# Kernel optimization log

Hardware: AMD Instinct MI355X
Metric: run time of the kernel (lower is better)

## Reference

```python
import jax, jax.numpy as jnp
import numpy as np


def setup_inputs() -> dict:
    key = jax.random.key(0)
    k1, k2, k3, k4 = jax.random.split(key, 4)
    N, F, E = 131072, 512, 256
    x = jax.random.normal(k1, (N, F), dtype=jnp.float32)
    W = jax.random.normal(k2, (E, F), dtype=jnp.float32) * 0.05  # stacked weak-classifier weights
    b = jax.random.normal(k3, (E,), dtype=jnp.float32) * 0.05
    alphas = jax.random.normal(k4, (E,), dtype=jnp.float32)
    return {"x": x, "W": W, "b": b, "alphas": alphas}


def reference(x, W, b, alphas):
    # Fused version of the per-estimator Python loop:
    # per estimator e: pred_e = round(sigmoid(x @ W[e] + b[e])) in {0,1}
    logits = jnp.einsum('nf,ef->ne', x, W) + b              # [N, E]
    preds = jnp.round(jax.nn.sigmoid(logits))               # [N, E], half-to-even like torch.round
    # original casts each (alpha * pred) term to long (trunc toward zero) before accumulating
    terms = jnp.trunc(alphas[None, :] * preds)              # [N, E]
    acc = jnp.sum(terms, axis=1)                            # [N]
    return jnp.sign(acc)
```

## Files before the change

### kernel.cpp

```cpp
#include <hip/hip_runtime.h>
#include <math.h>


#define F_DIM  512
#define BM     128
#define BK     32
#define KSTEPS 16
#define NT     8
#define WSLOTS 256
#define TAU    1e-3f

typedef float f32x4  __attribute__((ext_vector_type(4)));
typedef short bf16x8 __attribute__((ext_vector_type(8)));

__device__ inline unsigned short bf16_rne(float v) {
    unsigned u = __float_as_uint(v);
    u += 0x7FFFu + ((u >> 16) & 1u);
    return (unsigned short)(u >> 16);
}
__device__ inline float bf16_to_f32(unsigned short h) {
    return __uint_as_float(((unsigned)h) << 16);
}

__device__ inline void cvt8(const f32x4 a, const f32x4 b, bf16x8& hi, bf16x8& lo) {
    #pragma unroll
    for (int j = 0; j < 4; ++j) {
        const float v0 = a[j], v1 = b[j];
        const unsigned short h0 = bf16_rne(v0);
        const unsigned short h1 = bf16_rne(v1);
        hi[j]     = (short)h0;
        hi[j + 4] = (short)h1;
        lo[j]     = (short)bf16_rne(v0 - bf16_to_f32(h0));
        lo[j + 4] = (short)bf16_rne(v1 - bf16_to_f32(h1));
    }
}

__device__ __attribute__((noinline)) bool exact_pred(const float* __restrict__ xr,
                                                     const float* __restrict__ wr,
                                                     float bv) {
    double s0 = 0.0, s1 = 0.0, s2 = 0.0, s3 = 0.0;
    for (int k = 0; k < F_DIM; k += 4) {
        s0 = fma((double)xr[k + 0], (double)wr[k + 0], s0);
        s1 = fma((double)xr[k + 1], (double)wr[k + 1], s1);
        s2 = fma((double)xr[k + 2], (double)wr[k + 2], s2);
        s3 = fma((double)xr[k + 3], (double)wr[k + 3], s3);
    }
    double s = ((s0 + s1) + (s2 + s3)) + (double)bv;
    return s > 0.0;
}

__global__ __launch_bounds__(256)
void ada_prep(const float* __restrict__ W, const float* __restrict__ alphas,
              unsigned short* __restrict__ wfrag) {
    __shared__ int se[WSLOTS];
    __shared__ int wcnt[4];
    const int tid = threadIdx.x;

    se[tid] = 0;
    __syncthreads();
    const float t = truncf(alphas[tid]);
    const bool flag = (t != 0.0f);
    const unsigned long long m64 = __ballot(flag);
    const int lane = tid & 63, wvi = tid >> 6;
    if (lane == 0) wcnt[wvi] = __popcll(m64);
    __syncthreads();
    int off = 0;
    #pragma unroll
    for (int w = 0; w < 4; ++w) if (w < wvi) off += wcnt[w];
    if (flag) se[off + __popcll(m64 & ((1ull << lane) - 1ull))] = tid;
    __syncthreads();

    const int job = blockIdx.x * 256 + tid;
    const int jl  = job & 63;
    const int t8  = (job >> 6) & 7;
    const int ks  = (job >> 9) & 15;
    const int p   = (job >> 13) & 1;
    const int col = p * 128 + t8 * 16 + (jl & 15);
    const int k   = ks * 32 + (jl >> 4) * 8;

    const float* src = W + (size_t)se[col] * F_DIM + k;
    const f32x4 a = *(const f32x4*)(src);
    const f32x4 b = *(const f32x4*)(src + 4);
    bf16x8 hi, lo;
    cvt8(a, b, hi, lo);

    const size_t base = ((((size_t)(p * 16 + ks) * 8 + t8) * 2 + 0) * 64 + jl) * 8;
    *(bf16x8*)(wfrag + base)       = hi;
    *(bf16x8*)(wfrag + base + 512) = lo;
}

__global__ __launch_bounds__(256, 2)
void ada_mfma4(const float* __restrict__ x, const float* __restrict__ W,
               const float* __restrict__ bias, const float* __restrict__ alphas,
               const unsigned short* __restrict__ wfrag,
               float* __restrict__ out) {
    __shared__ unsigned short wbuf[2][8192];
    __shared__ int   se[WSLOTS];
    __shared__ float st[WSLOTS];
    __shared__ float sb[WSLOTS];
    __shared__ int   wcnt[4];

    const int tid = threadIdx.x;
    const int n0  = blockIdx.x * BM;

    se[tid] = 0; st[tid] = 0.0f; sb[tid] = 0.0f;
    __syncthreads();
    const float t = truncf(alphas[tid]);
    const bool flag = (t != 0.0f);
    const unsigned long long m64 = __ballot(flag);
    const int lane = tid & 63, wv = tid >> 6;
    if (lane == 0) wcnt[wv] = __popcll(m64);
    __syncthreads();
    int off = 0;
    #pragma unroll
    for (int w = 0; w < 4; ++w) if (w < wv) off += wcnt[w];
    const int M = wcnt[0] + wcnt[1] + wcnt[2] + wcnt[3];
    if (flag) {
        const int slot = off + __popcll(m64 & ((1ull << lane) - 1ull));
        se[slot] = tid; st[slot] = t; sb[slot] = bias[tid];
    }
    __syncthreads();

    const int quad = (tid >> 4) & 3;
    const int l15  = tid & 15;
    const int rw   = wv * 32;

    const float* xp0 = x + (size_t)(n0 + rw + l15) * F_DIM + quad * 8;
    const float* xp1 = xp0 + (size_t)16 * F_DIM;

    int part[2][4];
    #pragma unroll
    for (int mt = 0; mt < 2; ++mt)
        #pragma unroll
        for (int r = 0; r < 4; ++r) part[mt][r] = 0;

    for (int cb = 0; cb < M; cb += 128) {
        const unsigned short* wsp = wfrag + (size_t)(cb >> 7) * KSTEPS * 8192;

        f32x4 acc[2][NT];
        #pragma unroll
        for (int mt = 0; mt < 2; ++mt)
            #pragma unroll
            for (int nt = 0; nt < NT; ++nt)
                acc[mt][nt] = (f32x4){0.0f, 0.0f, 0.0f, 0.0f};

        {
            const unsigned short* gs = wsp + wv * 2048 + lane * 8;
            unsigned short* lb = &wbuf[0][wv * 2048];
            #pragma unroll
            for (int i = 0; i < 4; ++i)
                __builtin_amdgcn_global_load_lds(
                    (const __attribute__((address_space(1))) void*)(gs + i * 512),
                    (__attribute__((address_space(3))) void*)(lb + i * 512),
                    16, 0, 0);
        }
        f32x4 xv0 = *(const f32x4*)(xp0);
        f32x4 xv1 = *(const f32x4*)(xp0 + 4);
        f32x4 xv2 = *(const f32x4*)(xp1);
        f32x4 xv3 = *(const f32x4*)(xp1 + 4);
        __syncthreads();

        #pragma unroll
        for (int ks = 0; ks < KSTEPS; ++ks) {
            const int cur = ks & 1;

            f32x4 xn0, xn1, xn2, xn3;
            if (ks + 1 < KSTEPS) {
                const unsigned short* gs = wsp + (size_t)(ks + 1) * 8192 + wv * 2048 + lane * 8;
                unsigned short* lb = &wbuf[cur ^ 1][wv * 2048];
                #pragma unroll
                for (int i = 0; i < 4; ++i)
                    __builtin_amdgcn_global_load_lds(
                        (const __attribute__((address_space(1))) void*)(gs + i * 512),
                        (__attribute__((address_space(3))) void*)(lb + i * 512),
                        16, 0, 0);
                const int kf = (ks + 1) * BK;
                xn0 = *(const f32x4*)(xp0 + kf);
                xn1 = *(const f32x4*)(xp0 + kf + 4);
                xn2 = *(const f32x4*)(xp1 + kf);
                xn3 = *(const f32x4*)(xp1 + kf + 4);
            }

            bf16x8 ah0, al0, ah1, al1;
            cvt8(xv0, xv1, ah0, al0);
            cvt8(xv2, xv3, ah1, al1);

            const unsigned short* wb = wbuf[cur];
            #pragma unroll
            for (int nt = 0; nt < NT; ++nt) {
                const bf16x8 bh = *(const bf16x8*)&wb[(nt * 2 + 0) * 512 + lane * 8];
                const bf16x8 bl = *(const bf16x8*)&wb[(nt * 2 + 1) * 512 + lane * 8];
                acc[0][nt] = __builtin_amdgcn_mfma_f32_16x16x32_bf16(ah0, bh, acc[0][nt], 0, 0, 0);
                acc[1][nt] = __builtin_amdgcn_mfma_f32_16x16x32_bf16(ah1, bh, acc[1][nt], 0, 0, 0);
                acc[0][nt] = __builtin_amdgcn_mfma_f32_16x16x32_bf16(al0, bh, acc[0][nt], 0, 0, 0);
                acc[1][nt] = __builtin_amdgcn_mfma_f32_16x16x32_bf16(al1, bh, acc[1][nt], 0, 0, 0);
                acc[0][nt] = __builtin_amdgcn_mfma_f32_16x16x32_bf16(ah0, bl, acc[0][nt], 0, 0, 0);
                acc[1][nt] = __builtin_amdgcn_mfma_f32_16x16x32_bf16(ah1, bl, acc[1][nt], 0, 0, 0);
            }

            __syncthreads();

            if (ks + 1 < KSTEPS) { xv0 = xn0; xv1 = xn1; xv2 = xn2; xv3 = xn3; }
        }

        #pragma unroll
        for (int nt = 0; nt < NT; ++nt) {
            const int col = cb + nt * 16 + l15;
            const float tv = st[col];
            if (tv != 0.0f) {
                const float bv = sb[col];
                const int it = (int)tv;
                #pragma unroll
                for (int mt = 0; mt < 2; ++mt) {
                    #pragma unroll
                    for (int r = 0; r < 4; ++r) {
                        const float logit = acc[mt][nt][r] + bv;
                        bool pred = (logit > 0.0f);
                        if (fabsf(logit) < TAU) {
                            const int row = rw + mt * 16 + quad * 4 + r;
                            pred = exact_pred(x + (size_t)(n0 + row) * F_DIM,
                                              W + (size_t)se[col] * F_DIM, bv);
                        }
                        if (pred) part[mt][r] += it;
                    }
                }
            }
        }
    }

    #pragma unroll
    for (int mt = 0; mt < 2; ++mt) {
        #pragma unroll
        for (int r = 0; r < 4; ++r) {
            int v = part[mt][r];
            v += __shfl_xor(v, 1);
            v += __shfl_xor(v, 2);
            v += __shfl_xor(v, 4);
            v += __shfl_xor(v, 8);
            part[mt][r] = v;
        }
    }
    if (l15 == 0) {
        #pragma unroll
        for (int mt = 0; mt < 2; ++mt) {
            float4 o;
            o.x = (part[mt][0] > 0) ? 1.0f : (part[mt][0] < 0 ? -1.0f : 0.0f);
            o.y = (part[mt][1] > 0) ? 1.0f : (part[mt][1] < 0 ? -1.0f : 0.0f);
            o.z = (part[mt][2] > 0) ? 1.0f : (part[mt][2] < 0 ? -1.0f : 0.0f);
            o.w = (part[mt][3] > 0) ? 1.0f : (part[mt][3] < 0 ? -1.0f : 0.0f);
            *(float4*)(out + n0 + rw + mt * 16 + quad * 4) = o;
        }
    }
}

extern "C" void kernel_launch(void* const* d_in, const int* in_sizes, int n_in,
                              void* d_out, int out_size, void* d_ws, size_t ws_size,
                              hipStream_t stream) {
    const float* x      = (const float*)d_in[0];
    const float* W      = (const float*)d_in[1];
    const float* bias   = (const float*)d_in[2];
    const float* alphas = (const float*)d_in[3];
    float* out = (float*)d_out;

    const int n = in_sizes[0] / F_DIM;
    const int nblocks = n / BM;

    unsigned short* wfrag = (unsigned short*)d_ws;

    ada_prep<<<dim3(64), dim3(256), 0, stream>>>(W, alphas, wfrag);
    ada_mfma4<<<dim3(nblocks), dim3(256), 0, stream>>>(x, W, bias, alphas, wfrag, out);
}
```

Measured before the change: 549.7 us.

## Defer near-threshold exact recomputation to a separate fixup kernel via record list

Instead of calling a noinline double-precision dot product inline in the GEMM epilogue when a logit is near zero, the main kernel now writes raw integer votes and appends ambiguous (row, estimator, pred) records through an atomic counter. A separate fixup kernel recomputes those records exactly and corrects votes atomically, and a final kernel applies sign. This removes divergence and register pressure from the hot kernel, at the cost of two extra launches, global atomics, and a capped record buffer that could drop corrections if overflowed. The x bf16 conversion is also moved to the loop top to simplify the prefetch registers.

```diff
diff --git a/kernel.cpp b/kernel.cpp
--- a/kernel.cpp
+++ b/kernel.cpp
@@ -9,6 +9,7 @@
 #define NT     8
 #define WSLOTS 256
 #define TAU    1e-3f
+#define RECCAP 65536
 
 typedef float f32x4  __attribute__((ext_vector_type(4)));
 typedef short bf16x8 __attribute__((ext_vector_type(8)));
@@ -35,26 +36,14 @@
     }
 }
 
-__device__ __attribute__((noinline)) bool exact_pred(const float* __restrict__ xr,
-                                                     const float* __restrict__ wr,
-                                                     float bv) {
-    double s0 = 0.0, s1 = 0.0, s2 = 0.0, s3 = 0.0;
-    for (int k = 0; k < F_DIM; k += 4) {
-        s0 = fma((double)xr[k + 0], (double)wr[k + 0], s0);
-        s1 = fma((double)xr[k + 1], (double)wr[k + 1], s1);
-        s2 = fma((double)xr[k + 2], (double)wr[k + 2], s2);
-        s3 = fma((double)xr[k + 3], (double)wr[k + 3], s3);
-    }
-    double s = ((s0 + s1) + (s2 + s3)) + (double)bv;
-    return s > 0.0;
-}
-
 __global__ __launch_bounds__(256)
 void ada_prep(const float* __restrict__ W, const float* __restrict__ alphas,
-              unsigned short* __restrict__ wfrag) {
+              unsigned short* __restrict__ wfrag, int* __restrict__ cnt) {
     __shared__ int se[WSLOTS];
     __shared__ int wcnt[4];
     const int tid = threadIdx.x;
+
+    if (blockIdx.x == 0 && tid == 0) *cnt = 0;
 
     se[tid] = 0;
     __syncthreads();
@@ -90,10 +79,11 @@
 }
 
 __global__ __launch_bounds__(256, 2)
-void ada_mfma4(const float* __restrict__ x, const float* __restrict__ W,
+void ada_mfma6(const float* __restrict__ x,
                const float* __restrict__ bias, const float* __restrict__ alphas,
                const unsigned short* __restrict__ wfrag,
-               float* __restrict__ out) {
+               int* __restrict__ votes, int* __restrict__ cnt,
+               int* __restrict__ rec) {
     __shared__ unsigned short wbuf[2][8192];
     __shared__ int   se[WSLOTS];
     __shared__ float st[WSLOTS];
@@ -154,17 +144,20 @@
                     (__attribute__((address_space(3))) void*)(lb + i * 512),
                     16, 0, 0);
         }
-        f32x4 xv0 = *(const f32x4*)(xp0);
-        f32x4 xv1 = *(const f32x4*)(xp0 + 4);
-        f32x4 xv2 = *(const f32x4*)(xp1);
-        f32x4 xv3 = *(const f32x4*)(xp1 + 4);
+        f32x4 xn0 = *(const f32x4*)(xp0);
+        f32x4 xn1 = *(const f32x4*)(xp0 + 4);
+        f32x4 xn2 = *(const f32x4*)(xp1);
+        f32x4 xn3 = *(const f32x4*)(xp1 + 4);
         __syncthreads();
 
         #pragma unroll
         for (int ks = 0; ks < KSTEPS; ++ks) {
             const int cur = ks & 1;
 
-            f32x4 xn0, xn1, xn2, xn3;
+            bf16x8 ah0, al0, ah1, al1;
+            cvt8(xn0, xn1, ah0, al0);
+            cvt8(xn2, xn3, ah1, al1);
+
             if (ks + 1 < KSTEPS) {
                 const unsigned short* gs = wsp + (size_t)(ks + 1) * 8192 + wv * 2048 + lane * 8;
                 unsigned short* lb = &wbuf[cur ^ 1][wv * 2048];
@@ -181,10 +174,6 @@
                 xn3 = *(const f32x4*)(xp1 + kf + 4);
             }
 
-            bf16x8 ah0, al0, ah1, al1;
-            cvt8(xv0, xv1, ah0, al0);
-            cvt8(xv2, xv3, ah1, al1);
-
             const unsigned short* wb = wbuf[cur];
             #pragma unroll
             for (int nt = 0; nt < NT; ++nt) {
@@ -199,29 +188,28 @@
             }
 
             __syncthreads();
-
-            if (ks + 1 < KSTEPS) { xv0 = xn0; xv1 = xn1; xv2 = xn2; xv3 = xn3; }
         }
 
         #pragma unroll
         for (int nt = 0; nt < NT; ++nt) {
             const int col = cb + nt * 16 + l15;
             const float tv = st[col];
-            if (tv != 0.0f) {
-                const float bv = sb[col];
-                const int it = (int)tv;
+            const float bv = sb[col];
+            const int it = (int)tv;
+            #pragma unroll
+            for (int mt = 0; mt < 2; ++mt) {
                 #pragma unroll
-                for (int mt = 0; mt < 2; ++mt) {
-                    #pragma unroll
-                    for (int r = 0; r < 4; ++r) {
-                        const float logit = acc[mt][nt][r] + bv;
-                        bool pred = (logit > 0.0f);
+                for (int r = 0; r < 4; ++r) {
+                    const float logit = acc[mt][nt][r] + bv;
+                    const bool pred = (logit > 0.0f);
+                    if (tv != 0.0f) {
+                        if (pred) part[mt][r] += it;
                         if (fabsf(logit) < TAU) {
-                            const int row = rw + mt * 16 + quad * 4 + r;
-                            pred = exact_pred(x + (size_t)(n0 + row) * F_DIM,
-                                              W + (size_t)se[col] * F_DIM, bv);
+                            const int row = n0 + rw + mt * 16 + quad * 4 + r;
+                            const int idx = atomicAdd(cnt, 1);
+                            if (idx < RECCAP)
+                                rec[idx] = (row << 9) | (se[col] << 1) | (pred ? 1 : 0);
                         }
-                        if (pred) part[mt][r] += it;
                     }
                 }
             }
@@ -243,13 +231,57 @@
     if (l15 == 0) {
         #pragma unroll
         for (int mt = 0; mt < 2; ++mt) {
-            float4 o;
-            o.x = (part[mt][0] > 0) ? 1.0f : (part[mt][0] < 0 ? -1.0f : 0.0f);
-            o.y = (part[mt][1] > 0) ? 1.0f : (part[mt][1] < 0 ? -1.0f : 0.0f);
-            o.z = (part[mt][2] > 0) ? 1.0f : (part[mt][2] < 0 ? -1.0f : 0.0f);
-            o.w = (part[mt][3] > 0) ? 1.0f : (part[mt][3] < 0 ? -1.0f : 0.0f);
-            *(float4*)(out + n0 + rw + mt * 16 + quad * 4) = o;
-        }
+            int4 o;
+            o.x = part[mt][0]; o.y = part[mt][1];
+            o.z = part[mt][2]; o.w = part[mt][3];
+            *(int4*)(votes + n0 + rw + mt * 16 + quad * 4) = o;
+        }
+    }
+}
+
+__global__ __launch_bounds__(256)
+void ada_fix(const float* __restrict__ x, const float* __restrict__ W,
+             const float* __restrict__ bias, const float* __restrict__ alphas,
+             int* __restrict__ votes, const int* __restrict__ cnt,
+             const int* __restrict__ rec) {
+    int n = *cnt;
+    if (n > RECCAP) n = RECCAP;
+    const int stride = gridDim.x * blockDim.x;
+    for (int i = blockIdx.x * blockDim.x + threadIdx.x; i < n; i += stride) {
+        const int r    = rec[i];
+        const int row  = r >> 9;
+        const int e    = (r >> 1) & 255;
+        const int pred = r & 1;
+
+        const float* xr = x + (size_t)row * F_DIM;
+        const float* wr = W + (size_t)e * F_DIM;
+        double s0 = 0.0, s1 = 0.0, s2 = 0.0, s3 = 0.0;
+        for (int k = 0; k < F_DIM; k += 4) {
+            s0 = fma((double)xr[k + 0], (double)wr[k + 0], s0);
+            s1 = fma((double)xr[k + 1], (double)wr[k + 1], s1);
+            s2 = fma((double)xr[k + 2], (double)wr[k + 2], s2);
+            s3 = fma((double)xr[k + 3], (double)wr[k + 3], s3);
+        }
+        const double s = ((s0 + s1) + (s2 + s3)) + (double)bias[e];
+        const int q = (s > 0.0) ? 1 : 0;
+        if (q != pred) {
+            const int it = (int)truncf(alphas[e]);
+            atomicAdd(&votes[row], q ? it : -it);
+        }
+    }
+}
+
+__global__ __launch_bounds__(256)
+void ada_sign(const int* __restrict__ votes, float* __restrict__ out, int n4) {
+    const int i = blockIdx.x * blockDim.x + threadIdx.x;
+    if (i < n4) {
+        const int4 v = *(const int4*)(votes + i * 4);
+        float4 o;
+        o.x = (v.x > 0) ? 1.0f : (v.x < 0 ? -1.0f : 0.0f);
+        o.y = (v.y > 0) ? 1.0f : (v.y < 0 ? -1.0f : 0.0f);
+        o.z = (v.z > 0) ? 1.0f : (v.z < 0 ? -1.0f : 0.0f);
+        o.w = (v.w > 0) ? 1.0f : (v.w < 0 ? -1.0f : 0.0f);
+        *(float4*)(out + i * 4) = o;
     }
 }
 
@@ -265,8 +297,14 @@
     const int n = in_sizes[0] / F_DIM;
     const int nblocks = n / BM;
 
-    unsigned short* wfrag = (unsigned short*)d_ws;
-
-    ada_prep<<<dim3(64), dim3(256), 0, stream>>>(W, alphas, wfrag);
-    ada_mfma4<<<dim3(nblocks), dim3(256), 0, stream>>>(x, W, bias, alphas, wfrag, out);
-}
+    char* wsb = (char*)d_ws;
+    unsigned short* wfrag = (unsigned short*)wsb;
+    int* votes = (int*)(wsb + (512u << 10));
+    int* cnt   = (int*)(wsb + (1024u << 10));
+    int* rec   = (int*)(wsb + (1024u << 10) + 256);
+
+    ada_prep<<<dim3(64), dim3(256), 0, stream>>>(W, alphas, wfrag, cnt);
+    ada_mfma6<<<dim3(nblocks), dim3(256), 0, stream>>>(x, bias, alphas, wfrag, votes, cnt, rec);
+    ada_fix<<<dim3(32), dim3(256), 0, stream>>>(x, W, bias, alphas, votes, cnt, rec);
+    ada_sign<<<dim3(n / 1024), dim3(256), 0, stream>>>(votes, out, n / 4);
+}
```

New measurement: 508.4 us. -7.5%, faster.
